# Performance work log

Measured on AMD Instinct MI355X. Metric: run time of the kernel, lower is better.

The kernel has to match this reference:

```python
import jax, jax.numpy as jnp
import numpy as np

KH, KW = 3, 3
K = KH * KW
PAD, STRIDE, DIL = 1, 1, 1


def _conv(x, w, b):
    y = jax.lax.conv_general_dilated(
        x, w, (STRIDE, STRIDE), ((PAD, PAD), (PAD, PAD)),
        rhs_dilation=(DIL, DIL), dimension_numbers=('NCHW', 'OIHW', 'NCHW'))
    return y + b[None, :, None, None]


def _bilinear_gather(x, py, px):
    # x: [B,C,H,W]; py, px: float sample coords [B,K,Ho,Wo]. Zero outside bounds.
    B, C, H, W = x.shape
    y0 = jnp.floor(py)
    x0 = jnp.floor(px)
    wy1 = py - y0
    wx1 = px - x0
    wy0 = 1.0 - wy1
    wx0 = 1.0 - wx1
    xf = x.reshape(B, C, H * W)

    def g(yi, xi):
        valid = (yi >= 0) & (yi < H) & (xi >= 0) & (xi < W)
        yc = jnp.clip(yi, 0, H - 1).astype(jnp.int32)
        xc = jnp.clip(xi, 0, W - 1).astype(jnp.int32)
        idx = (yc * W + xc).reshape(B, -1)                      # [B, K*Ho*Wo]
        v = jax.vmap(lambda im, ix: im[:, ix])(xf, idx)         # [B, C, K*Ho*Wo]
        v = v.reshape(B, C, *yi.shape[1:])                      # [B,C,K,Ho,Wo]
        return v * valid[:, None].astype(x.dtype)

    return ((wy0 * wx0)[:, None] * g(y0, x0)
            + (wy0 * wx1)[:, None] * g(y0, x0 + 1)
            + (wy1 * wx0)[:, None] * g(y0 + 1, x0)
            + (wy1 * wx1)[:, None] * g(y0 + 1, x0 + 1))


def setup_inputs() -> dict:
    key = jax.random.key(0)
    k1, k2, k3 = jax.random.split(key, 3)
    B, C, H, W = 8, 256, 64, 64
    x = jax.random.normal(k1, (B, C, H, W), dtype=jnp.float32)
    # small init for offset/mask conv so predicted offsets stay modest (as in DCNv2 practice)
    w_om = jax.random.normal(k2, (3 * K, C, KH, KW), dtype=jnp.float32) * 0.01
    b_om = jnp.zeros((3 * K,), dtype=jnp.float32)
    w_dc = jax.random.normal(k3, (C, C, KH, KW), dtype=jnp.float32) * (1.0 / np.sqrt(C * K))
    b_dc = jnp.zeros((C,), dtype=jnp.float32)
    return {"x": x, "w_om": w_om, "b_om": b_om, "w_dc": w_dc, "b_dc": b_dc}


def reference(x, w_om, b_om, w_dc, b_dc):
    B, C, H, W = x.shape
    om = _conv(x, w_om, b_om)                      # [B, 3K, H, W]
    offset = om[:, :2 * K].reshape(B, K, 2, H, W)  # per-tap (dy, dx)
    mask = jax.nn.sigmoid(om[:, 2 * K:])           # [B, K, H, W]
    dy, dx = offset[:, :, 0], offset[:, :, 1]
    kh = jnp.repeat(jnp.arange(KH), KW)            # [K] kernel row index
    kw = jnp.tile(jnp.arange(KW), KH)              # [K] kernel col index
    ho = jnp.arange(H)
    wo = jnp.arange(W)
    py = ho[None, None, :, None] * STRIDE - PAD + kh[None, :, None, None] * DIL + dy
    px = wo[None, None, None, :] * STRIDE - PAD + kw[None, :, None, None] * DIL + dx
    sampled = _bilinear_gather(x, py, px)          # [B,C,K,H,W]
    sampled = sampled * mask[:, None]              # modulated (DCNv2)
    w = w_dc.reshape(w_dc.shape[0], C, K)
    out = jnp.einsum('bckhw,ock->bohw', sampled, w) + b_dc[None, :, None, None]
    return out
```

## Files before the change

### kernel.cpp

```cpp
#include <hip/hip_runtime.h>
#include <hip/hip_bf16.h>
#include <math.h>

#define BB   8
#define CIN  256
#define HH   64
#define WW   64
#define OMC  27
#define HW   (HH*WW)
#define KTOT (CIN*9)
#define NPIX 32
#define SPITCH 296
#define TCOLS  40
#define TCH5   200
#define NST5   25
#define XP1    40

typedef short bf16x8 __attribute__((ext_vector_type(8)));
typedef float f32x4  __attribute__((ext_vector_type(4)));

__device__ __forceinline__ unsigned short f2bf(float f) {
    union { float f; unsigned int u; } v; v.f = f;
    unsigned int r = v.u + 0x7FFFu + ((v.u >> 16) & 1u);
    return (unsigned short)(r >> 16);
}

#define GLOAD_LDS16(g, l) __builtin_amdgcn_global_load_lds( \
    (const __attribute__((address_space(1))) void*)(g),     \
    (__attribute__((address_space(3))) void*)(l), 16, 0, 0)

__global__ __launch_bounds__(256) void wprep_kernel(
    const float* __restrict__ w_dc, unsigned short* __restrict__ wA)
{
    int e = blockIdx.x * 256 + threadIdx.x;
    int o = e / KTOT;
    int k = e - o * KTOT;
    int c   = k / 9;
    int tap = k - c * 9;
    int kp  = (c >> 5) * 288 + tap * 32 + (c & 31);
    wA[((size_t)(kp >> 3) * 256 + o) * 8 + (kp & 7)] = f2bf(w_dc[e]);
}

__global__ __launch_bounds__(256) void womprep_kernel(
    const float* __restrict__ w_om, unsigned short* __restrict__ wOmA)
{
    int e = blockIdx.x * 256 + threadIdx.x;
    int j  = e & 7;
    int t1 = e >> 3;
    int o  = t1 & 31;
    int t2 = t1 >> 5;
    int cb = t2 & 3;
    int t3 = t2 >> 2;
    int cc = t3 & 7;
    int tap = t3 >> 3;
    int c = cc * 32 + cb * 8 + j;
    float v = (o < OMC) ? w_om[(size_t)o * KTOT + c * 9 + tap] : 0.f;
    wOmA[e] = f2bf(v);
}

__global__ __launch_bounds__(512, 6) void deform_mfma_kernel(
    const float* __restrict__ x, const unsigned short* __restrict__ wOmA,
    const float* __restrict__ b_om,
    const unsigned short* __restrict__ wA, const float* __restrict__ b_dc,
    float* __restrict__ out)
{
    const int bid  = blockIdx.x;
    const int b    = bid >> 7;
    const int h    = (bid >> 1) & 63;
    const int w0   = (bid & 1) * NPIX;
    const int t    = threadIdx.x;
    const int wv   = t >> 6;
    const int lane = t & 63;
    const int lq   = lane >> 4;
    const int lm   = lane & 15;

    __shared__ __align__(16) unsigned short sS[NPIX * SPITCH];
    __shared__ __align__(16) float sT[32 * TCH5 + 64];
    __shared__ int    s_lbp[9 * NPIX];
    __shared__ float4 s_w4 [9 * NPIX];

    float* som  = reinterpret_cast<float*>(s_w4);
    unsigned short* bufA = reinterpret_cast<unsigned short*>(sT);
    unsigned short* bufB = bufA + 4080;

    const size_t xb_base = (size_t)b * CIN * HW;
    const float* gx_base = x + xb_base;

    int srcOff5[4];
#pragma unroll
    for (int i = 0; i < 4; ++i) {
        int wi = wv + i * 8;
        int q  = wi * 64 + lane;
        if (wi < NST5) {
            int ch  = q / 50;
            int rem = q - ch * 50;
            int row = rem / 10;
            int c4  = rem - row * 10;
            int gy  = min(max(h - 2 + row, 0), HH - 1);
            int gx0 = min(max(w0 - 4 + c4 * 4, 0), WW - 4);
            srcOff5[i] = ch * HW + gy * WW + gx0;
        } else srcOff5[i] = 0;
    }

    {
        f32x4 accOm = (f32x4)(0.f);
        const int mfp = (wv >> 1) & 1;
        const int nfp = wv & 1;
        const int p   = nfp * 16 + lm;
        const bf16x8* wOmV = reinterpret_cast<const bf16x8*>(wOmA);

        auto stage1 = [&](int cc, unsigned short* dst) {
            const float* gch = gx_base + (size_t)cc * 32 * HW;
#pragma unroll
            for (int i = 0; i < 7; ++i) {
                int e = t + i * 512;
                if (e < 3264) {
                    int cl  = e / 102;
                    int rc  = e - cl * 102;
                    int row = rc / 34;
                    int col = rc - row * 34;
                    int gy  = h - 1 + row;
                    int gxx = w0 - 1 + col;
                    float v = 0.f;
                    if (gy >= 0 && gy < HH && (unsigned)gxx < WW)
                        v = gch[cl * HW + gy * WW + gxx];
                    dst[rc * XP1 + cl] = f2bf(v);
                }
            }
        };

        stage1(0, bufA);
        __syncthreads();
        for (int cc = 0; cc < 8; ++cc) {
            unsigned short* cur = (cc & 1) ? bufB : bufA;
            unsigned short* nxt = (cc & 1) ? bufA : bufB;
            if (cc < 7) stage1(cc + 1, nxt);
#pragma unroll
            for (int tap = 0; tap < 9; ++tap) {
                int kh = tap / 3, kw = tap % 3;
                bf16x8 bfr = *reinterpret_cast<const bf16x8*>(
                    &cur[(kh * 34 + p + kw) * XP1 + lq * 8]);
                bf16x8 af = wOmV[(((tap * 8 + cc) * 4 + lq) * 32) + mfp * 16 + lm];
                accOm = __builtin_amdgcn_mfma_f32_16x16x32_bf16(af, bfr, accOm, 0, 0, 0);
            }
            __syncthreads();
        }

        if (wv < 4) {
#pragma unroll
            for (int r = 0; r < 4; ++r) {
                int o = mfp * 16 + lq * 4 + r;
                if (o < OMC)
                    som[o * NPIX + p] = accOm[r] + b_om[o];
            }
        }
    }
    __syncthreads();

#pragma unroll
    for (int i = 0; i < 4; ++i)
        if (wv + i * 8 < NST5)
            GLOAD_LDS16(gx_base + srcOff5[i], (char*)sT + (wv + i * 8) * 1024);
    __builtin_amdgcn_sched_barrier(0);

    int   p_pk = 0;
    float4 p_w4 = make_float4(0.f, 0.f, 0.f, 0.f);
    if (t < 9 * NPIX) {
        int tap = t >> 5;
        int pix = t & 31;
        float dy = som[(2 * tap) * NPIX + pix];
        float dx = som[(2 * tap + 1) * NPIX + pix];
        float mv = som[(18 + tap) * NPIX + pix];
        float m  = 1.f / (1.f + expf(-mv));
        float py = (float)(h - 1 + tap / 3) + dy;
        float px = (float)(w0 + pix - 1 + tap % 3) + dx;
        float y0f = floorf(py), x0f = floorf(px);
        float wy1 = py - y0f, wx1 = px - x0f;
        float wy0 = 1.f - wy1, wx0 = 1.f - wx1;
        int y0 = (int)y0f, x0 = (int)x0f;
        int y1 = y0 + 1, x1 = x0 + 1;
        bool yv0 = (y0 >= 0) && (y0 < HH);
        bool yv1 = (y1 >= 0) && (y1 < HH);
        bool xv0 = (x0 >= 0) && (x0 < WW);
        bool xv1 = (x1 >= 0) && (x1 < WW);
        int yc0 = min(max(y0, 0), HH - 1), yc1 = min(max(y1, 0), HH - 1);
        int xc0 = min(max(x0, 0), WW - 1), xc1 = min(max(x1, 0), WW - 1);
        p_w4.x = (yv0 && xv0) ? wy0 * wx0 * m : 0.f;
        p_w4.y = (yv0 && xv1) ? wy0 * wx1 * m : 0.f;
        p_w4.z = (yv1 && xv0) ? wy1 * wx0 * m : 0.f;
        p_w4.w = (yv1 && xv1) ? wy1 * wx1 * m : 0.f;
        if (xc1 == xc0) { p_w4.x += p_w4.y; p_w4.y = 0.f;
                          p_w4.z += p_w4.w; p_w4.w = 0.f; }
        if (yc1 == yc0) { p_w4.x += p_w4.z; p_w4.z = 0.f;
                          p_w4.y += p_w4.w; p_w4.w = 0.f; }
        bool inT = (yc0 >= h - 2) && (yc1 <= h + 2) &&
                   (xc0 >= w0 - 4) && (xc1 <= w0 + 35);
        int lb = (yc0 - (h - 2)) * TCOLS + (xc0 - (w0 - 4));
        p_pk = (lb & 0xFF) | ((xc1 - xc0) << 8) | ((yc1 - yc0) << 9)
             | ((yc0 * WW + xc0) << 10);
        if (!inT) p_pk |= (int)0x80000000;
    }
    if (t >= 448) sT[32 * TCH5 + (t - 448)] = 0.f;
    __syncthreads();
    if (t < 9 * NPIX) {
        s_lbp[t] = p_pk;
        s_w4[t]  = p_w4;
    }
    __syncthreads();

    f32x4 acc[2][2];
#pragma unroll
    for (int i = 0; i < 2; ++i)
#pragma unroll
        for (int j = 0; j < 2; ++j)
            acc[i][j] = (f32x4)(0.f);

    const int pix  = t & 31;
    const int slot = t >> 5;
    const int clb2 = slot * 2;

    for (int ch = 0; ch < 8; ++ch) {
#pragma unroll 3
        for (int tap = 0; tap < 9; ++tap) {
            int    idx = tap * NPIX + pix;
            int    pk  = s_lbp[idx];
            float4 ww  = s_w4[idx];
            float v0, v1;
            if (pk >= 0) {
                const float* pp = &sT[clb2 * TCH5 + (pk & 0xFF)];
                v0 = ww.x * pp[0]     + ww.y * pp[1]
                   + ww.z * pp[TCOLS] + ww.w * pp[TCOLS + 1];
                const float* qq = pp + TCH5;
                v1 = ww.x * qq[0]     + ww.y * qq[1]
                   + ww.z * qq[TCOLS] + ww.w * qq[TCOLS + 1];
            } else {
                int off00 = (pk >> 10) & 0xFFF;
                int d01 = (pk >> 8) & 1;
                int d10 = ((pk >> 9) & 1) * WW;
                int d11 = d10 + d01;
                const float* xc = x + xb_base + (size_t)(ch * 32 + clb2) * HW;
                v0 = ww.x * xc[off00]       + ww.y * xc[off00 + d01]
                   + ww.z * xc[off00 + d10] + ww.w * xc[off00 + d11];
                xc += HW;
                v1 = ww.x * xc[off00]       + ww.y * xc[off00 + d01]
                   + ww.z * xc[off00 + d10] + ww.w * xc[off00 + d11];
            }
            *reinterpret_cast<unsigned int*>(&sS[pix * SPITCH + tap * 32 + clb2]) =
                f2bf(v0) | ((unsigned int)f2bf(v1) << 16);
        }
        __syncthreads();

        if (ch < 7) {
            const float* gb = gx_base + (size_t)(ch + 1) * 32 * HW;
#pragma unroll
            for (int i = 0; i < 4; ++i)
                if (wv + i * 8 < NST5)
                    GLOAD_LDS16(gb + srcOff5[i], (char*)sT + (wv + i * 8) * 1024);
            __builtin_amdgcn_sched_barrier(0);
        }

        const int kb_base = ch * 36;
        const bf16x8* wAv = reinterpret_cast<const bf16x8*>(wA);
#pragma unroll 1
        for (int ks = 0; ks < 9; ++ks) {
            bf16x8 bfr[2];
#pragma unroll
            for (int nf = 0; nf < 2; ++nf)
                bfr[nf] = *reinterpret_cast<const bf16x8*>(
                    &sS[(nf * 16 + lm) * SPITCH + ks * 32 + lq * 8]);
#pragma unroll
            for (int mf = 0; mf < 2; ++mf) {
                int o  = wv * 32 + mf * 16 + lm;
                int kb = kb_base + ks * 4 + lq;
                bf16x8 af = wAv[(size_t)kb * 256 + o];
#pragma unroll
                for (int nf = 0; nf < 2; ++nf)
                    acc[mf][nf] = __builtin_amdgcn_mfma_f32_16x16x32_bf16(
                        af, bfr[nf], acc[mf][nf], 0, 0, 0);
            }
        }
        __syncthreads();
    }

#pragma unroll
    for (int mf = 0; mf < 2; ++mf) {
#pragma unroll
        for (int r = 0; r < 4; ++r) {
            int o = wv * 32 + mf * 16 + lq * 4 + r;
            float bo = b_dc[o];
#pragma unroll
            for (int nf = 0; nf < 2; ++nf) {
                int p = nf * 16 + lm;
                out[((size_t)(b * 256 + o)) * HW + h * WW + w0 + p] = acc[mf][nf][r] + bo;
            }
        }
    }
}

extern "C" void kernel_launch(void* const* d_in, const int* in_sizes, int n_in,
                              void* d_out, int out_size, void* d_ws, size_t ws_size,
                              hipStream_t stream) {
    const float* x    = (const float*)d_in[0];
    const float* w_om = (const float*)d_in[1];
    const float* b_om = (const float*)d_in[2];
    const float* w_dc = (const float*)d_in[3];
    const float* b_dc = (const float*)d_in[4];
    float* out = (float*)d_out;

    unsigned short* wA   = (unsigned short*)d_ws;
    unsigned short* wOmA = (unsigned short*)((char*)d_ws + 1179648);

    wprep_kernel<<<(256 * KTOT) / 256, 256, 0, stream>>>(w_dc, wA);
    womprep_kernel<<<73728 / 256, 256, 0, stream>>>(w_om, wOmA);
    deform_mfma_kernel<<<BB * HH * 2, 512, 0, stream>>>(x, wOmA, b_om, wA, b_dc, out);
}
```

Baseline: 181.0 us.

## Stage input tile as packed bf16 channel pairs in LDS via register prefetch

```diff
diff --git a/kernel.cpp b/kernel.cpp
--- a/kernel.cpp
+++ b/kernel.cpp
@@ -1,5 +1,6 @@
 #include <hip/hip_runtime.h>
 #include <hip/hip_bf16.h>
+#include <hip/hip_fp16.h>
 #include <math.h>
 
 #define BB   8
@@ -11,10 +12,8 @@
 #define KTOT (CIN*9)
 #define NPIX 32
 #define SPITCH 296
-#define TCOLS  40
-#define TCH5   200
-#define NST5   25
 #define XP1    40
+#define TPW    17
 
 typedef short bf16x8 __attribute__((ext_vector_type(8)));
 typedef float f32x4  __attribute__((ext_vector_type(4)));
@@ -24,10 +23,12 @@
     unsigned int r = v.u + 0x7FFFu + ((v.u >> 16) & 1u);
     return (unsigned short)(r >> 16);
 }
-
-#define GLOAD_LDS16(g, l) __builtin_amdgcn_global_load_lds( \
-    (const __attribute__((address_space(1))) void*)(g),     \
-    (__attribute__((address_space(3))) void*)(l), 16, 0, 0)
+__device__ __forceinline__ float bflo(unsigned int a) {
+    union { unsigned int u; float f; } c; c.u = a << 16; return c.f;
+}
+__device__ __forceinline__ float bfhi(unsigned int a) {
+    union { unsigned int u; float f; } c; c.u = a & 0xFFFF0000u; return c.f;
+}
 
 __global__ __launch_bounds__(256) void wprep_kernel(
     const float* __restrict__ w_dc, unsigned short* __restrict__ wA)
@@ -58,7 +59,7 @@
     wOmA[e] = f2bf(v);
 }
 
-__global__ __launch_bounds__(512, 6) void deform_mfma_kernel(
+__global__ __launch_bounds__(512, 8) void deform_mfma_kernel(
     const float* __restrict__ x, const unsigned short* __restrict__ wOmA,
     const float* __restrict__ b_om,
     const unsigned short* __restrict__ wA, const float* __restrict__ b_dc,
@@ -75,31 +76,30 @@
     const int lm   = lane & 15;
 
     __shared__ __align__(16) unsigned short sS[NPIX * SPITCH];
-    __shared__ __align__(16) float sT[32 * TCH5 + 64];
-    __shared__ int    s_lbp[9 * NPIX];
-    __shared__ float4 s_w4 [9 * NPIX];
-
-    float* som  = reinterpret_cast<float*>(s_w4);
-    unsigned short* bufA = reinterpret_cast<unsigned short*>(sT);
-    unsigned short* bufB = bufA + 4080;
+    __shared__ __align__(16) unsigned short sR[8224];
+    __shared__ int     s_lbp[9 * NPIX];
+    __shared__ __half2 s_wp [9 * NPIX * 2];
+
+    float* som  = reinterpret_cast<float*>(sS);
+    unsigned short* bufA = sR;
+    unsigned short* bufB = sR + 4080;
 
     const size_t xb_base = (size_t)b * CIN * HW;
     const float* gx_base = x + xb_base;
 
-    int srcOff5[4];
-#pragma unroll
-    for (int i = 0; i < 4; ++i) {
-        int wi = wv + i * 8;
-        int q  = wi * 64 + lane;
-        if (wi < NST5) {
-            int ch  = q / 50;
-            int rem = q - ch * 50;
-            int row = rem / 10;
-            int c4  = rem - row * 10;
-            int gy  = min(max(h - 2 + row, 0), HH - 1);
-            int gx0 = min(max(w0 - 4 + c4 * 4, 0), WW - 4);
-            srcOff5[i] = ch * HW + gy * WW + gx0;
-        } else srcOff5[i] = 0;
+    int stg[7];
+#pragma unroll
+    for (int i = 0; i < 7; ++i) {
+        int n = t + i * 512;
+        if (n < 3200) {
+            int slot = n / 200;
+            int rc   = n - slot * 200;
+            int r    = rc / 40;
+            int c    = rc - r * 40;
+            int gy   = min(max(h - 2 + r, 0), HH - 1);
+            int gx   = min(max(w0 - 4 + c, 0), WW - 1);
+            stg[i] = (rc * TPW + slot) | (slot << 12) | ((gy * WW + gx) << 16);
+        } else stg[i] = -1;
     }
 
     {
@@ -157,14 +157,24 @@
     }
     __syncthreads();
 
-#pragma unroll
-    for (int i = 0; i < 4; ++i)
-        if (wv + i * 8 < NST5)
-            GLOAD_LDS16(gx_base + srcOff5[i], (char*)sT + (wv + i * 8) * 1024);
-    __builtin_amdgcn_sched_barrier(0);
-
-    int   p_pk = 0;
-    float4 p_w4 = make_float4(0.f, 0.f, 0.f, 0.f);
+    float L0[7], L1[7];
+    {
+        const float* gch = gx_base;
+#pragma unroll
+        for (int i = 0; i < 7; ++i)
+            if (stg[i] >= 0) {
+                int sl = (stg[i] >> 12) & 0xF;
+                int go = (stg[i] >> 16) & 0xFFF;
+                L0[i] = gch[(size_t)(2 * sl) * HW + go];
+                L1[i] = gch[(size_t)(2 * sl + 1) * HW + go];
+            }
+    }
+
+    {
+        unsigned int* tWw = reinterpret_cast<unsigned int*>(sR);
+        for (int i = t; i < 712; i += 512) tWw[3400 + i] = 0u;
+    }
+
     if (t < 9 * NPIX) {
         int tap = t >> 5;
         int pix = t & 31;
@@ -185,26 +195,29 @@
         bool xv1 = (x1 >= 0) && (x1 < WW);
         int yc0 = min(max(y0, 0), HH - 1), yc1 = min(max(y1, 0), HH - 1);
         int xc0 = min(max(x0, 0), WW - 1), xc1 = min(max(x1, 0), WW - 1);
-        p_w4.x = (yv0 && xv0) ? wy0 * wx0 * m : 0.f;
-        p_w4.y = (yv0 && xv1) ? wy0 * wx1 * m : 0.f;
-        p_w4.z = (yv1 && xv0) ? wy1 * wx0 * m : 0.f;
-        p_w4.w = (yv1 && xv1) ? wy1 * wx1 * m : 0.f;
-        if (xc1 == xc0) { p_w4.x += p_w4.y; p_w4.y = 0.f;
-                          p_w4.z += p_w4.w; p_w4.w = 0.f; }
-        if (yc1 == yc0) { p_w4.x += p_w4.z; p_w4.z = 0.f;
-                          p_w4.y += p_w4.w; p_w4.w = 0.f; }
+        float wwx = (yv0 && xv0) ? wy0 * wx0 * m : 0.f;
+        float wwy = (yv0 && xv1) ? wy0 * wx1 * m : 0.f;
+        float wwz = (yv1 && xv0) ? wy1 * wx0 * m : 0.f;
+        float www = (yv1 && xv1) ? wy1 * wx1 * m : 0.f;
+        if (xc1 == xc0) { wwx += wwy; wwy = 0.f; wwz += www; www = 0.f; }
+        if (yc1 == yc0) { wwx += wwz; wwz = 0.f; wwy += www; www = 0.f; }
         bool inT = (yc0 >= h - 2) && (yc1 <= h + 2) &&
                    (xc0 >= w0 - 4) && (xc1 <= w0 + 35);
-        int lb = (yc0 - (h - 2)) * TCOLS + (xc0 - (w0 - 4));
-        p_pk = (lb & 0xFF) | ((xc1 - xc0) << 8) | ((yc1 - yc0) << 9)
-             | ((yc0 * WW + xc0) << 10);
-        if (!inT) p_pk |= (int)0x80000000;
-    }
-    if (t >= 448) sT[32 * TCH5 + (t - 448)] = 0.f;
-    __syncthreads();
-    if (t < 9 * NPIX) {
-        s_lbp[t] = p_pk;
-        s_w4[t]  = p_w4;
+        int lb = (yc0 - (h - 2)) * 40 + (xc0 - (w0 - 4));
+        int pk = (lb & 0xFF) | ((xc1 - xc0) << 8) | ((yc1 - yc0) << 9)
+               | ((yc0 * WW + xc0) << 10);
+        if (!inT) pk |= (int)0x80000000;
+        s_lbp[t] = pk;
+        s_wp[2 * t]     = __floats2half2_rn(wwx, wwy);
+        s_wp[2 * t + 1] = __floats2half2_rn(wwz, www);
+    }
+    {
+        unsigned int* tWw = reinterpret_cast<unsigned int*>(sR);
+#pragma unroll
+        for (int i = 0; i < 7; ++i)
+            if (stg[i] >= 0)
+                tWw[stg[i] & 0xFFF] =
+                    f2bf(L0[i]) | ((unsigned int)f2bf(L1[i]) << 16);
     }
     __syncthreads();
 
@@ -215,48 +228,55 @@
         for (int j = 0; j < 2; ++j)
             acc[i][j] = (f32x4)(0.f);
 
-    const int pix  = t & 31;
-    const int slot = t >> 5;
-    const int clb2 = slot * 2;
+    const int pix  = t >> 4;
+    const int slot = t & 15;
+    const unsigned int* tW = reinterpret_cast<const unsigned int*>(sR);
 
     for (int ch = 0; ch < 8; ++ch) {
 #pragma unroll 3
         for (int tap = 0; tap < 9; ++tap) {
-            int    idx = tap * NPIX + pix;
-            int    pk  = s_lbp[idx];
-            float4 ww  = s_w4[idx];
+            int idx = tap * NPIX + pix;
+            int pk  = s_lbp[idx];
+            float2 wab = __half22float2(s_wp[2 * idx]);
+            float2 wcd = __half22float2(s_wp[2 * idx + 1]);
             float v0, v1;
             if (pk >= 0) {
-                const float* pp = &sT[clb2 * TCH5 + (pk & 0xFF)];
-                v0 = ww.x * pp[0]     + ww.y * pp[1]
-                   + ww.z * pp[TCOLS] + ww.w * pp[TCOLS + 1];
-                const float* qq = pp + TCH5;
-                v1 = ww.x * qq[0]     + ww.y * qq[1]
-                   + ww.z * qq[TCOLS] + ww.w * qq[TCOLS + 1];
+                int base = (pk & 0xFF) * TPW + slot;
+                unsigned int a00 = tW[base];
+                unsigned int a01 = tW[base + TPW];
+                unsigned int a10 = tW[base + 40 * TPW];
+                unsigned int a11 = tW[base + 41 * TPW];
+                v0 = wab.x * bflo(a00) + wab.y * bflo(a01)
+                   + wcd.x * bflo(a10) + wcd.y * bflo(a11);
+                v1 = wab.x * bfhi(a00) + wab.y * bfhi(a01)
+                   + wcd.x * bfhi(a10) + wcd.y * bfhi(a11);
             } else {
                 int off00 = (pk >> 10) & 0xFFF;
                 int d01 = (pk >> 8) & 1;
                 int d10 = ((pk >> 9) & 1) * WW;
-                int d11 = d10 + d01;
-                const float* xc = x + xb_base + (size_t)(ch * 32 + clb2) * HW;
-                v0 = ww.x * xc[off00]       + ww.y * xc[off00 + d01]
-                   + ww.z * xc[off00 + d10] + ww.w * xc[off00 + d11];
+                const float* xc = x + xb_base + (size_t)(ch * 32 + 2 * slot) * HW;
+                v0 = wab.x * xc[off00]       + wab.y * xc[off00 + d01]
+                   + wcd.x * xc[off00 + d10] + wcd.y * xc[off00 + d10 + d01];
                 xc += HW;
-                v1 = ww.x * xc[off00]       + ww.y * xc[off00 + d01]
-                   + ww.z * xc[off00 + d10] + ww.w * xc[off00 + d11];
-            }
-            *reinterpret_cast<unsigned int*>(&sS[pix * SPITCH + tap * 32 + clb2]) =
+                v1 = wab.x * xc[off00]       + wab.y * xc[off00 + d01]
+                   + wcd.x * xc[off00 + d10] + wcd.y * xc[off00 + d10 + d01];
+            }
+            *reinterpret_cast<unsigned int*>(
+                &sS[pix * SPITCH + tap * 32 + 2 * slot]) =
                 f2bf(v0) | ((unsigned int)f2bf(v1) << 16);
         }
         __syncthreads();
 
         if (ch < 7) {
-            const float* gb = gx_base + (size_t)(ch + 1) * 32 * HW;
-#pragma unroll
-            for (int i = 0; i < 4; ++i)
-                if (wv + i * 8 < NST5)
-                    GLOAD_LDS16(gb + srcOff5[i], (char*)sT + (wv + i * 8) * 1024);
-            __builtin_amdgcn_sched_barrier(0);
+            const float* gch = gx_base + (size_t)(ch + 1) * 32 * HW;
+#pragma unroll
+            for (int i = 0; i < 7; ++i)
+                if (stg[i] >= 0) {
+                    int sl = (stg[i] >> 12) & 0xF;
+                    int go = (stg[i] >> 16) & 0xFFF;
+                    L0[i] = gch[(size_t)(2 * sl) * HW + go];
+                    L1[i] = gch[(size_t)(2 * sl + 1) * HW + go];
+                }
         }
 
         const int kb_base = ch * 36;
@@ -278,6 +298,15 @@
                     acc[mf][nf] = __builtin_amdgcn_mfma_f32_16x16x32_bf16(
                         af, bfr[nf], acc[mf][nf], 0, 0, 0);
             }
+        }
+
+        if (ch < 7) {
+            unsigned int* tWw = reinterpret_cast<unsigned int*>(sR);
+#pragma unroll
+            for (int i = 0; i < 7; ++i)
+                if (stg[i] >= 0)
+                    tWw[stg[i] & 0xFFF] =
+                        f2bf(L0[i]) | ((unsigned int)f2bf(L1[i]) << 16);
         }
         __syncthreads();
     }
```

New measurement: 208.7 us. 15.3% more time.
